# Performance work log

Hardware: AMD Instinct MI355X
Metric: run time of the kernel (lower is better)

Reference implementation:

```python
import jax, jax.numpy as jnp
import numpy as np

DIM = 256
NUM_HEADS = 8
WINDOW = 7


def setup_inputs() -> dict:
    key = jax.random.key(0)
    ks = jax.random.split(key, 6)
    B, N, C = 4, 2048, DIM
    x = jax.random.normal(ks[0], (B, N, C), dtype=jnp.float32)
    qkv_w = jax.random.normal(ks[1], (3 * C, C), dtype=jnp.float32) * 0.02
    qkv_b = jax.random.normal(ks[2], (3 * C,), dtype=jnp.float32) * 0.02
    proj_w = jax.random.normal(ks[3], (C, C), dtype=jnp.float32) * 0.02
    proj_b = jax.random.normal(ks[4], (C,), dtype=jnp.float32) * 0.02
    bias_table = jax.random.normal(ks[5], ((2 * WINDOW - 1) * NUM_HEADS,), dtype=jnp.float32) * 0.02
    return {"x": x, "qkv_w": qkv_w, "qkv_b": qkv_b, "proj_w": proj_w,
            "proj_b": proj_b, "bias_table": bias_table}


def _rel_bias(bias_table, seq_len):
    w = WINDOW
    coords = jnp.arange(w)
    idx = coords[:, None] - coords[None, :] + (w - 1)  # (w, w), values in [0, 2w-2]
    # Faithful to original: table[idx.view(-1)].view(w,w,-1) -> last dim 1,
    # i.e. bias is shared across heads.
    bias = bias_table[idx]  # (w, w)
    if seq_len <= w:
        return bias[:seq_len, :seq_len]
    repeats = (seq_len + w - 1) // w
    bias = jnp.tile(bias, (repeats, repeats))[:seq_len, :seq_len]
    return bias  # (N, N)


def reference(x, qkv_w, qkv_b, proj_w, proj_b, bias_table):
    B, N, C = x.shape
    H, hd = NUM_HEADS, C // NUM_HEADS
    qkv = x @ qkv_w.T + qkv_b                       # (B, N, 3C)
    qkv = qkv.reshape(B, N, 3, H, hd).transpose(2, 0, 3, 1, 4)
    q, k, v = qkv[0], qkv[1], qkv[2]                # each (B, H, N, hd)
    scale = hd ** -0.5
    attn = jnp.einsum('bhnd,bhmd->bhnm', q, k) * scale  # (B, H, N, N)
    bias = _rel_bias(bias_table, N)                 # (N, N), shared across heads
    attn = attn + bias[None, None, :, :]
    attn = jax.nn.softmax(attn, axis=-1)
    out = jnp.einsum('bhnm,bhmd->bhnd', attn, v)    # (B, H, N, hd)
    out = out.transpose(0, 2, 1, 3).reshape(B, N, C)
    return out @ proj_w.T + proj_b
```

## Files before the change

### kernel.cpp

```cpp
#include <hip/hip_runtime.h>
#include <stdint.h>

#define DIMC   256
#define NHEADS 8
#define HD     32
#define BATCH  4
#define SEQ    2048
#define MTOT   (BATCH * SEQ)
#define QKVN   (MTOT * HD * NHEADS)
#define SCALE  0.17677669529663687f
#define LOG2E  1.4426950408889634f
#define SCL2E  (SCALE * LOG2E)

typedef short bf16x8 __attribute__((ext_vector_type(8)));
typedef float f32x4  __attribute__((ext_vector_type(4)));

#if defined(__has_builtin)
#if __has_builtin(__builtin_amdgcn_exp2f)
#define EXP2F __builtin_amdgcn_exp2f
#else
#define EXP2F exp2f
#endif
#else
#define EXP2F exp2f
#endif

static __device__ __forceinline__ unsigned short f2bf(float f) {
    unsigned int u = __float_as_uint(f);
    u += 0x7fffu + ((u >> 16) & 1u);
    return (unsigned short)(u >> 16);
}

static __device__ __forceinline__ unsigned int cvt2(float a, float b) {
#if defined(__has_builtin) && __has_builtin(__builtin_amdgcn_cvt_pk_bf16_f32)
    typedef __bf16 bf2 __attribute__((ext_vector_type(2)));
    bf2 v = __builtin_amdgcn_cvt_pk_bf16_f32(a, b);
    return __builtin_bit_cast(unsigned int, v);
#else
    return (unsigned int)f2bf(a) | ((unsigned int)f2bf(b) << 16);
#endif
}

#define NX8   262144
#define NWQ8  24576
#define NWP8  8192
#define NQA8  8192
#define NKA8  8192
#define NPREP (NX8 + NWQ8 + NWP8 + NQA8 + NKA8)

__global__ __launch_bounds__(256) void prep_kernel(
    const float* __restrict__ x, const float* __restrict__ wq,
    const float* __restrict__ wp, const float* __restrict__ table,
    unsigned short* __restrict__ xbf, unsigned short* __restrict__ wqbf,
    unsigned short* __restrict__ wpbf,
    unsigned short* __restrict__ QA, unsigned short* __restrict__ KA)
{
    int g = blockIdx.x * 256 + threadIdx.x;
    const float* src = nullptr;
    unsigned short* dst = nullptr;
    if (g < NX8)                      { src = x  + (size_t)g * 8;            dst = xbf  + (size_t)g * 8; }
    else if (g < NX8 + NWQ8)          { int l = g - NX8;        src = wq + (size_t)l * 8; dst = wqbf + (size_t)l * 8; }
    else if (g < NX8 + NWQ8 + NWP8)   { int l = g - NX8 - NWQ8; src = wp + (size_t)l * 8; dst = wpbf + (size_t)l * 8; }
    if (src) {
        float4 a0 = *(const float4*)src;
        float4 a1 = *(const float4*)(src + 4);
        uint4 pk;
        pk.x = cvt2(a0.x, a0.y); pk.y = cvt2(a0.z, a0.w);
        pk.z = cvt2(a1.x, a1.y); pk.w = cvt2(a1.z, a1.w);
        *(uint4*)dst = pk;
        return;
    }
    int l = g - (NX8 + NWQ8 + NWP8);
    if (l < NQA8) {
        int row = l >> 2, i0 = (l & 3) << 3, r7 = row % 7;
        unsigned short v[8];
        #pragma unroll
        for (int i = 0; i < 8; i++) v[i] = (i0 + i == r7) ? (unsigned short)0x3F80 : (unsigned short)0;
        *(uint4*)(QA + (size_t)row * 32 + i0) = *(const uint4*)v;
    } else if (l < NQA8 + NKA8) {
        l -= NQA8;
        int row = l >> 2, i0 = (l & 3) << 3, r7 = row % 7;
        unsigned short v[8];
        #pragma unroll
        for (int i = 0; i < 8; i++) {
            int ii = i0 + i;
            v[i] = (ii < 7) ? f2bf(table[ii - r7 + 6] * LOG2E) : (unsigned short)0;
        }
        *(uint4*)(KA + (size_t)row * 32 + i0) = *(const uint4*)v;
    }
}

template<int MODE>
__global__ __launch_bounds__(256) void gemm_mfma_kernel(
    const unsigned short* __restrict__ A,
    const unsigned short* __restrict__ W,
    const float* __restrict__ bias,
    unsigned short* __restrict__ qb,
    unsigned short* __restrict__ kb,
    unsigned short* __restrict__ vtb,
    float* __restrict__ outf)
{
    __shared__ unsigned short FW[8][64][32];

    const int t    = threadIdx.x;
    const int wave = t >> 6;
    const int lane = t & 63;
    const int cg   = lane & 15;
    const int quad = lane >> 4;
    const int m0   = blockIdx.y * 64;
    const int n0   = blockIdx.x * 64;

    {
        int r = t >> 2, c8 = (t & 3) << 3;
        #pragma unroll
        for (int chunk = 0; chunk < 8; chunk++)
            *(bf16x8*)&FW[chunk][r][c8] =
                *(const bf16x8*)(W + (size_t)(n0 + r) * 256 + chunk * 32 + c8);
    }
    __syncthreads();

    const unsigned short* Arow = A + (size_t)(m0 + wave * 16 + cg) * 256 + quad * 8;

    f32x4 acc[4];
    #pragma unroll
    for (int c = 0; c < 4; c++) acc[c] = (f32x4){0.f, 0.f, 0.f, 0.f};

    #pragma unroll
    for (int chunk = 0; chunk < 8; chunk++) {
        bf16x8 af = *(const bf16x8*)(Arow + chunk * 32);
        bf16x8 wf[4];
        #pragma unroll
        for (int c = 0; c < 4; c++)
            wf[c] = *(const bf16x8*)&FW[chunk][c * 16 + cg][quad * 8];
        #pragma unroll
        for (int c = 0; c < 4; c++)
            acc[c] = __builtin_amdgcn_mfma_f32_16x16x32_bf16(af, wf[c], acc[c], 0, 0, 0);
    }

    #pragma unroll
    for (int c = 0; c < 4; c++) {
        int n = n0 + c * 16 + cg;
        float bv = bias[n];
        #pragma unroll
        for (int rr = 0; rr < 4; rr++) {
            int m = m0 + wave * 16 + quad * 4 + rr;
            float val = acc[c][rr] + bv;
            if (MODE == 0) {
                int which = n >> 8;
                int h     = (n >> 5) & 7;
                int d     = n & 31;
                int b_    = m >> 11;
                int nn    = m & 2047;
                int bh    = b_ * NHEADS + h;
                if (which == 0)
                    qb[((size_t)bh * SEQ + nn) * HD + d] = f2bf(val * SCL2E);
                else if (which == 1)
                    kb[((size_t)bh * SEQ + nn) * HD + d] = f2bf(val);
                else
                    vtb[((size_t)bh * HD + d) * SEQ + nn] = f2bf(val);
            } else {
                outf[(size_t)m * 256 + n] = val;
            }
        }
    }
}

__global__ __launch_bounds__(256) void attn_mfma_kernel(
    const unsigned short* __restrict__ Q,
    const unsigned short* __restrict__ K,
    const unsigned short* __restrict__ Vt,
    const unsigned short* __restrict__ QA,
    const unsigned short* __restrict__ KA,
    unsigned short* __restrict__ AO)
{
    __shared__ unsigned short PL[4][64][72];

    const int t    = threadIdx.x;
    const int wave = t >> 6;
    const int lane = t & 63;
    const int cg   = lane & 15;
    const int quad = lane >> 4;

    const int bid = blockIdx.x;
    const int qt  = bid & 31;
    const int bh  = bid >> 5;
    const int b   = bh >> 3;
    const int h   = bh & 7;
    const int q0  = qt * 64;

    const unsigned short* Kbase = K  + (size_t)bh * (SEQ * HD);
    const unsigned short* Vbase = Vt + (size_t)bh * (SEQ * HD);

    bf16x8 qf[4], qfa[4];
    #pragma unroll
    for (int qi = 0; qi < 4; qi++) {
        qf[qi]  = *(const bf16x8*)(Q + (size_t)bh * (SEQ * HD) +
                                   (size_t)(q0 + qi * 16 + cg) * HD + quad * 8);
        qfa[qi] = *(const bf16x8*)(QA + (size_t)(q0 + qi * 16 + cg) * HD + quad * 8);
    }

    f32x4 o[4][2];
    float rs[4];
    #pragma unroll
    for (int qi = 0; qi < 4; qi++) {
        o[qi][0] = (f32x4){0.f, 0.f, 0.f, 0.f};
        o[qi][1] = (f32x4){0.f, 0.f, 0.f, 0.f};
        rs[qi] = 0.f;
    }

    const int kstart = wave * (SEQ / 4);
    for (int jj = 0; jj < SEQ / 4; jj += 64) {
        const int j0 = kstart + jj;

        bf16x8 kf[4], kfa[4];
        #pragma unroll
        for (int jt = 0; jt < 4; jt++) {
            kf[jt]  = *(const bf16x8*)(Kbase + (size_t)(j0 + jt * 16 + cg) * HD + quad * 8);
            kfa[jt] = *(const bf16x8*)(KA    + (size_t)(j0 + jt * 16 + cg) * HD + quad * 8);
        }
        bf16x8 vf[2][2];
        #pragma unroll
        for (int kt = 0; kt < 2; kt++)
            #pragma unroll
            for (int dt = 0; dt < 2; dt++)
                vf[kt][dt] = *(const bf16x8*)(Vbase + (size_t)(dt * 16 + cg) * SEQ +
                                              j0 + kt * 32 + quad * 8);

        #pragma unroll
        for (int half = 0; half < 2; half++) {
            f32x4 s[2][4];
            #pragma unroll
            for (int qh = 0; qh < 2; qh++) {
                int qi = half * 2 + qh;
                #pragma unroll
                for (int jt = 0; jt < 4; jt++) {
                    s[qh][jt] = __builtin_amdgcn_mfma_f32_16x16x32_bf16(
                        kfa[jt], qfa[qi], (f32x4){0.f, 0.f, 0.f, 0.f}, 0, 0, 0);
                    s[qh][jt] = __builtin_amdgcn_mfma_f32_16x16x32_bf16(
                        kf[jt], qf[qi], s[qh][jt], 0, 0, 0);
                }
            }
            #pragma unroll
            for (int qh = 0; qh < 2; qh++) {
                int qi = half * 2 + qh;
                #pragma unroll
                for (int jt = 0; jt < 4; jt++) {
                    float p0 = EXP2F(s[qh][jt][0]);
                    float p1 = EXP2F(s[qh][jt][1]);
                    float p2 = EXP2F(s[qh][jt][2]);
                    float p3 = EXP2F(s[qh][jt][3]);
                    rs[qi] += (p0 + p1) + (p2 + p3);
                    uint2 w;
                    w.x = cvt2(p0, p1);
                    w.y = cvt2(p2, p3);
                    *(uint2*)&PL[wave][qi * 16 + cg][jt * 16 + quad * 4] = w;
                }
            }
        }
        __builtin_amdgcn_s_waitcnt(0xC07F);

        #pragma unroll
        for (int qi = 0; qi < 4; qi++) {
            bf16x8 pa0 = *(const bf16x8*)&PL[wave][qi * 16 + cg][quad * 8];
            bf16x8 pa1 = *(const bf16x8*)&PL[wave][qi * 16 + cg][32 + quad * 8];
            o[qi][0] = __builtin_amdgcn_mfma_f32_16x16x32_bf16(pa0, vf[0][0], o[qi][0], 0, 0, 0);
            o[qi][0] = __builtin_amdgcn_mfma_f32_16x16x32_bf16(pa1, vf[1][0], o[qi][0], 0, 0, 0);
            o[qi][1] = __builtin_amdgcn_mfma_f32_16x16x32_bf16(pa0, vf[0][1], o[qi][1], 0, 0, 0);
            o[qi][1] = __builtin_amdgcn_mfma_f32_16x16x32_bf16(pa1, vf[1][1], o[qi][1], 0, 0, 0);
        }
    }

    #pragma unroll
    for (int qi = 0; qi < 4; qi++) {
        rs[qi] += __shfl_xor(rs[qi], 16, 64);
        rs[qi] += __shfl_xor(rs[qi], 32, 64);
    }

    __builtin_amdgcn_s_waitcnt(0xC07F);
    float* OPw = (float*)&PL[wave][0][0];
    #pragma unroll
    for (int qi = 0; qi < 4; qi++) {
        #pragma unroll
        for (int dt = 0; dt < 2; dt++)
            #pragma unroll
            for (int rr = 0; rr < 4; rr++)
                OPw[(qi * 16 + quad * 4 + rr) * 33 + dt * 16 + cg] = o[qi][dt][rr];
        if (quad == 0)
            OPw[(qi * 16 + cg) * 33 + 32] = rs[qi];
    }
    __syncthreads();

    {
        int q  = t >> 2;
        int d0 = (t & 3) << 3;
        float l = 0.f;
        float ov[8];
        #pragma unroll
        for (int i = 0; i < 8; i++) ov[i] = 0.f;
        #pragma unroll
        for (int w = 0; w < 4; w++) {
            const float* OPx = (const float*)&PL[w][0][0];
            l += OPx[q * 33 + 32];
            #pragma unroll
            for (int i = 0; i < 8; i++) ov[i] += OPx[q * 33 + d0 + i];
        }
        float inv = 1.f / l;
        unsigned short pk[8];
        #pragma unroll
        for (int i = 0; i < 8; i += 2) {
            unsigned int u = cvt2(ov[i] * inv, ov[i + 1] * inv);
            pk[i]     = (unsigned short)(u & 0xffffu);
            pk[i + 1] = (unsigned short)(u >> 16);
        }
        *(uint4*)(AO + ((size_t)(b * SEQ + q0 + q)) * DIMC + h * HD + d0) = *(const uint4*)pk;
    }
}

extern "C" void kernel_launch(void* const* d_in, const int* in_sizes, int n_in,
                              void* d_out, int out_size, void* d_ws, size_t ws_size,
                              hipStream_t stream) {
    const float* x      = (const float*)d_in[0];
    const float* qkv_w  = (const float*)d_in[1];
    const float* qkv_b  = (const float*)d_in[2];
    const float* proj_w = (const float*)d_in[3];
    const float* proj_b = (const float*)d_in[4];
    const float* table  = (const float*)d_in[5];
    float* out = (float*)d_out;

    unsigned short* ws   = (unsigned short*)d_ws;
    unsigned short* qb   = ws;
    unsigned short* kb   = qb  + (size_t)QKVN;
    unsigned short* vtb  = kb  + (size_t)QKVN;
    unsigned short* ao   = vtb + (size_t)QKVN;
    unsigned short* xbf  = ao  + (size_t)QKVN;
    unsigned short* wqbf = xbf + (size_t)QKVN;
    unsigned short* wpbf = wqbf + 196608;
    unsigned short* QAt  = wpbf + 65536;
    unsigned short* KAt  = QAt  + 65536;

    prep_kernel<<<dim3((NPREP + 255) / 256), 256, 0, stream>>>(
        x, qkv_w, proj_w, table, xbf, wqbf, wpbf, QAt, KAt);

    gemm_mfma_kernel<0><<<dim3(768 / 64, MTOT / 64), 256, 0, stream>>>(
        xbf, wqbf, qkv_b, qb, kb, vtb, nullptr);

    attn_mfma_kernel<<<dim3(BATCH * NHEADS * (SEQ / 64)), 256, 0, stream>>>(
        qb, kb, vtb, QAt, KAt, ao);

    gemm_mfma_kernel<1><<<dim3(256 / 64, MTOT / 64), 256, 0, stream>>>(
        ao, wpbf, proj_b, nullptr, nullptr, nullptr, out);
}
```

Baseline: 138.9 us.

## Transpose V through shared memory for coalesced stores; compute softmax rowsum via MFMA

In the QKV GEMM, blocks producing V (blockIdx.x >= 8) now stage their output tile in shared memory transposed, then write packed 16-element bf16 vectors to the V-transposed buffer. This replaces scattered 2-byte strided stores. The FW tile is padded to 36 columns. The attention kernel drops the per-element VALU row-sum and shuffle reduction and instead accumulates row sums with extra MFMAs against a ones vector, which also sums the bf16-rounded probabilities. The KV loop is unrolled by 2, at the cost of more MFMA work and register pressure.

```diff
diff --git a/kernel.cpp b/kernel.cpp
--- a/kernel.cpp
+++ b/kernel.cpp
@@ -100,7 +100,9 @@
     unsigned short* __restrict__ vtb,
     float* __restrict__ outf)
 {
-    __shared__ unsigned short FW[8][64][32];
+    __shared__ unsigned char LSD[8 * 64 * 36 * 2];
+    unsigned short (*FW)[64][36] = (unsigned short (*)[64][36])LSD;
+    float (*TR)[65] = (float (*)[65])LSD;
 
     const int t    = threadIdx.x;
     const int wave = t >> 6;
@@ -135,6 +137,39 @@
         #pragma unroll
         for (int c = 0; c < 4; c++)
             acc[c] = __builtin_amdgcn_mfma_f32_16x16x32_bf16(af, wf[c], acc[c], 0, 0, 0);
+    }
+
+    if (MODE == 0 && blockIdx.x >= 8) {
+        __syncthreads();
+        #pragma unroll
+        for (int c = 0; c < 4; c++) {
+            int l = c * 16 + cg;
+            float bv = bias[n0 + l];
+            #pragma unroll
+            for (int rr = 0; rr < 4; rr++)
+                TR[l][wave * 16 + quad * 4 + rr] = acc[c][rr] + bv;
+        }
+        __syncthreads();
+        int l  = t >> 2;
+        int mm = (t & 3) << 4;
+        int n  = n0 + l;
+        int h  = (n >> 5) & 7;
+        int d  = n & 31;
+        int b_ = m0 >> 11;
+        int nn = (m0 & 2047) + mm;
+        float4 v0 = *(const float4*)&TR[l][mm];
+        float4 v1 = *(const float4*)&TR[l][mm + 4];
+        float4 v2 = *(const float4*)&TR[l][mm + 8];
+        float4 v3 = *(const float4*)&TR[l][mm + 12];
+        uint4 pk0, pk1;
+        pk0.x = cvt2(v0.x, v0.y); pk0.y = cvt2(v0.z, v0.w);
+        pk0.z = cvt2(v1.x, v1.y); pk0.w = cvt2(v1.z, v1.w);
+        pk1.x = cvt2(v2.x, v2.y); pk1.y = cvt2(v2.z, v2.w);
+        pk1.z = cvt2(v3.x, v3.y); pk1.w = cvt2(v3.z, v3.w);
+        unsigned short* dst = vtb + ((size_t)((b_ * NHEADS + h) * HD + d)) * SEQ + nn;
+        *(uint4*)dst       = pk0;
+        *(uint4*)(dst + 8) = pk1;
+        return;
     }
 
     #pragma unroll
@@ -154,10 +189,8 @@
                 int bh    = b_ * NHEADS + h;
                 if (which == 0)
                     qb[((size_t)bh * SEQ + nn) * HD + d] = f2bf(val * SCL2E);
-                else if (which == 1)
+                else
                     kb[((size_t)bh * SEQ + nn) * HD + d] = f2bf(val);
-                else
-                    vtb[((size_t)bh * HD + d) * SEQ + nn] = f2bf(val);
             } else {
                 outf[(size_t)m * 256 + n] = val;
             }
@@ -199,16 +232,20 @@
         qfa[qi] = *(const bf16x8*)(QA + (size_t)(q0 + qi * 16 + cg) * HD + quad * 8);
     }
 
-    f32x4 o[4][2];
-    float rs[4];
+    bf16x8 ones;
+    #pragma unroll
+    for (int i = 0; i < 8; i++) ones[i] = (short)0x3F80;
+
+    f32x4 o[4][2], ol[4];
     #pragma unroll
     for (int qi = 0; qi < 4; qi++) {
         o[qi][0] = (f32x4){0.f, 0.f, 0.f, 0.f};
         o[qi][1] = (f32x4){0.f, 0.f, 0.f, 0.f};
-        rs[qi] = 0.f;
+        ol[qi]   = (f32x4){0.f, 0.f, 0.f, 0.f};
     }
 
     const int kstart = wave * (SEQ / 4);
+    #pragma unroll 2
     for (int jj = 0; jj < SEQ / 4; jj += 64) {
         const int j0 = kstart + jj;
 
@@ -249,7 +286,6 @@
                     float p1 = EXP2F(s[qh][jt][1]);
                     float p2 = EXP2F(s[qh][jt][2]);
                     float p3 = EXP2F(s[qh][jt][3]);
-                    rs[qi] += (p0 + p1) + (p2 + p3);
                     uint2 w;
                     w.x = cvt2(p0, p1);
                     w.y = cvt2(p2, p3);
@@ -267,13 +303,9 @@
             o[qi][0] = __builtin_amdgcn_mfma_f32_16x16x32_bf16(pa1, vf[1][0], o[qi][0], 0, 0, 0);
             o[qi][1] = __builtin_amdgcn_mfma_f32_16x16x32_bf16(pa0, vf[0][1], o[qi][1], 0, 0, 0);
             o[qi][1] = __builtin_amdgcn_mfma_f32_16x16x32_bf16(pa1, vf[1][1], o[qi][1], 0, 0, 0);
-        }
-    }
-
-    #pragma unroll
-    for (int qi = 0; qi < 4; qi++) {
-        rs[qi] += __shfl_xor(rs[qi], 16, 64);
-        rs[qi] += __shfl_xor(rs[qi], 32, 64);
+            ol[qi]   = __builtin_amdgcn_mfma_f32_16x16x32_bf16(pa0, ones, ol[qi], 0, 0, 0);
+            ol[qi]   = __builtin_amdgcn_mfma_f32_16x16x32_bf16(pa1, ones, ol[qi], 0, 0, 0);
+        }
     }
 
     __builtin_amdgcn_s_waitcnt(0xC07F);
@@ -285,8 +317,11 @@
             #pragma unroll
             for (int rr = 0; rr < 4; rr++)
                 OPw[(qi * 16 + quad * 4 + rr) * 33 + dt * 16 + cg] = o[qi][dt][rr];
-        if (quad == 0)
-            OPw[(qi * 16 + cg) * 33 + 32] = rs[qi];
+        if (cg == 0) {
+            #pragma unroll
+            for (int rr = 0; rr < 4; rr++)
+                OPw[(qi * 16 + quad * 4 + rr) * 33 + 32] = ol[qi][rr];
+        }
     }
     __syncthreads();
 
```

Result: slower. 155.2 us (+11.8%).
